# Kernel tuning notes

Measured on AMD Instinct MI355X. Metric: run time of the kernel, lower is better.

## Reference

```python
import jax, jax.numpy as jnp
import numpy as np

B, L, INPUT_DIM = 2, 2048, 512
D_MODEL, N_HEAD, MLP_HIDDEN = 1024, 16, 4096
CONTEXT_LENGTH = 2048
EPS = 1e-5


def _layer_norm(x, w, b):
    mu = jnp.mean(x, axis=-1, keepdims=True)
    var = jnp.mean(jnp.square(x - mu), axis=-1, keepdims=True)
    return (x - mu) * jax.lax.rsqrt(var + EPS) * w + b


def setup_inputs() -> dict:
    key = jax.random.key(0)
    ks = jax.random.split(key, 12)
    s = 0.02
    return {
        "x": jax.random.normal(ks[0], (B, L, INPUT_DIM), dtype=jnp.float32),
        "wte_w": jax.random.normal(ks[1], (INPUT_DIM, D_MODEL), dtype=jnp.float32) * s,
        "wte_b": jnp.zeros((D_MODEL,), dtype=jnp.float32),
        "wpe": jax.random.normal(ks[2], (CONTEXT_LENGTH, D_MODEL), dtype=jnp.float32) * s,
        "ln1_w": jnp.ones((D_MODEL,), dtype=jnp.float32),
        "ln1_b": jnp.zeros((D_MODEL,), dtype=jnp.float32),
        "kq_w": jax.random.normal(ks[3], (D_MODEL, 2 * D_MODEL), dtype=jnp.float32) * s,
        "kq_b": jnp.zeros((2 * D_MODEL,), dtype=jnp.float32),
        "v_w": jax.random.normal(ks[4], (D_MODEL, D_MODEL), dtype=jnp.float32) * s,
        "v_b": jnp.zeros((D_MODEL,), dtype=jnp.float32),
        "ao_w": jax.random.normal(ks[5], (D_MODEL, D_MODEL), dtype=jnp.float32) * s,
        "ao_b": jnp.zeros((D_MODEL,), dtype=jnp.float32),
        "ln2_w": jnp.ones((D_MODEL,), dtype=jnp.float32),
        "ln2_b": jnp.zeros((D_MODEL,), dtype=jnp.float32),
        "fc_w": jax.random.normal(ks[6], (D_MODEL, MLP_HIDDEN), dtype=jnp.float32) * s,
        "fc_b": jnp.zeros((MLP_HIDDEN,), dtype=jnp.float32),
        "proj_w": jax.random.normal(ks[7], (MLP_HIDDEN, INPUT_DIM), dtype=jnp.float32) * s,
        "proj_b": jnp.zeros((INPUT_DIM,), dtype=jnp.float32),
    }


def reference(x, wte_w, wte_b, wpe, ln1_w, ln1_b, kq_w, kq_b, v_w, v_b,
              ao_w, ao_b, ln2_w, ln2_b, fc_w, fc_b, proj_w, proj_b):
    b, l, _ = x.shape
    hd = D_MODEL // N_HEAD
    # token "embedding" (linear) + learnable positional embedding
    h = x @ wte_w + wte_b + wpe[:l]                      # [B, L, D]
    hn = _layer_norm(h, ln1_w, ln1_b)                    # ln_1
    # attention (kq fused linear -> split gives k first, then q)
    kq = hn @ kq_w + kq_b                                # [B, L, 2D]
    k, q = kq[..., :D_MODEL], kq[..., D_MODEL:]
    v = hn @ v_w + v_b
    q = q.reshape(b, l, N_HEAD, hd).transpose(0, 2, 1, 3)  # [B, H, L, hd]
    k = k.reshape(b, l, N_HEAD, hd).transpose(0, 2, 1, 3)
    v = v.reshape(b, l, N_HEAD, hd).transpose(0, 2, 1, 3)
    scale = 1.0 / jnp.sqrt(jnp.asarray(hd, dtype=q.dtype))
    scores = jnp.einsum('bhqd,bhkd->bhqk', q, k) * scale  # [B, H, L, L]
    causal = jnp.tril(jnp.ones((l, l), dtype=bool))
    scores = jnp.where(causal, scores, jnp.asarray(-jnp.inf, dtype=scores.dtype))
    attn = jax.nn.softmax(scores, axis=-1)
    o = jnp.einsum('bhqk,bhkd->bhqd', attn, v)            # [B, H, L, hd]
    o = o.transpose(0, 2, 1, 3).reshape(b, l, D_MODEL)
    o = o @ ao_w + ao_b
    attn_out = hn + o                                     # residual recorded by Block
    xo = _layer_norm(attn_out, ln2_w, ln2_b)              # ln_2
    # MLP head to input_dim (exact GELU, matching torch nn.GELU default)
    out = jax.nn.gelu(xo @ fc_w + fc_b, approximate=False) @ proj_w + proj_b
    return (out, attn_out)
```

## Files before the change

### kernel.cpp

```cpp
#include <hip/hip_runtime.h>
#include <hip/hip_bf16.h>
#include <cmath>

#define D_MODEL   1024
#define N_HEAD    16
#define HEAD_DIM  64
#define SEQ_LEN   2048
#define NBATCH    2
#define M_TOTAL   (NBATCH * SEQ_LEN)
#define IN_DIM    512
#define MLP_HID   4096

typedef __attribute__((ext_vector_type(8))) short short8;
typedef __attribute__((ext_vector_type(4))) short short4v;
typedef __attribute__((ext_vector_type(4))) float floatx4;

typedef const __attribute__((address_space(1))) void* gas_ptr;
typedef __attribute__((address_space(3))) void* las_ptr;

__device__ __forceinline__ void async_copy16(const void* g, void* l) {
  __builtin_amdgcn_global_load_lds((gas_ptr)g, (las_ptr)l, 16, 0, 0);
}


__global__ __launch_bounds__(256) void k_prep(const float* __restrict__ wte_w,
                                              const float* __restrict__ kq_w,
                                              const float* __restrict__ v_w,
                                              const float* __restrict__ ao_w,
                                              const float* __restrict__ fc_w,
                                              const float* __restrict__ proj_w,
                                              const float* __restrict__ x,
                                              __hip_bfloat16* __restrict__ wT,
                                              __hip_bfloat16* __restrict__ x_bf) {
  const int bid = blockIdx.x;
  const float* in; __hip_bfloat16* out; int K, N, local;
  if (bid < 512)        { in = wte_w;  out = wT;           K = IN_DIM;  N = D_MODEL;     local = bid;        }
  else if (bid < 2560)  { in = kq_w;   out = wT +  524288; K = D_MODEL; N = 2 * D_MODEL; local = bid - 512;  }
  else if (bid < 3584)  { in = v_w;    out = wT + 2621440; K = D_MODEL; N = D_MODEL;     local = bid - 2560; }
  else if (bid < 4608)  { in = ao_w;   out = wT + 3670016; K = D_MODEL; N = D_MODEL;     local = bid - 3584; }
  else if (bid < 8704)  { in = fc_w;   out = wT + 4718592; K = D_MODEL; N = MLP_HID;     local = bid - 4608; }
  else if (bid < 10752) { in = proj_w; out = wT + 8912896; K = MLP_HID; N = IN_DIM;      local = bid - 8704; }
  else {
    int i = (bid - 10752) * 256 + threadIdx.x;
    float4 v = ((const float4*)x)[i];
    short4v o;
    ((__hip_bfloat16*)&o)[0] = __float2bfloat16(v.x);
    ((__hip_bfloat16*)&o)[1] = __float2bfloat16(v.y);
    ((__hip_bfloat16*)&o)[2] = __float2bfloat16(v.z);
    ((__hip_bfloat16*)&o)[3] = __float2bfloat16(v.w);
    ((short4v*)x_bf)[i] = o;
    return;
  }
  __shared__ float tile[32][33];
  const int ntx = N >> 5;
  const int bx = local % ntx, by = local / ntx;
  const int n0 = bx * 32, k0 = by * 32;
  const int tx = threadIdx.x & 31, ty = threadIdx.x >> 5;
#pragma unroll
  for (int i = 0; i < 32; i += 8)
    tile[ty + i][tx] = in[(size_t)(k0 + ty + i) * N + n0 + tx];
  __syncthreads();
#pragma unroll
  for (int i = 0; i < 32; i += 8)
    out[(size_t)(n0 + ty + i) * K + k0 + tx] = __float2bfloat16(tile[tx][ty + i]);
}

__global__ __launch_bounds__(256) void k_reduce_proj(const __hip_bfloat16* __restrict__ part,
                                                     const float* __restrict__ bias,
                                                     float* __restrict__ out) {
  int i = blockIdx.x * 256 + threadIdx.x;
  const size_t SP = (size_t)M_TOTAL * IN_DIM / 4;
  float4 s = ((const float4*)bias)[i & (IN_DIM / 4 - 1)];
#pragma unroll
  for (int j = 0; j < 8; j++) {
    short4v v = ((const short4v*)part)[i + j * SP];
    s.x += __bfloat162float(((const __hip_bfloat16*)&v)[0]);
    s.y += __bfloat162float(((const __hip_bfloat16*)&v)[1]);
    s.z += __bfloat162float(((const __hip_bfloat16*)&v)[2]);
    s.w += __bfloat162float(((const __hip_bfloat16*)&v)[3]);
  }
  ((float4*)out)[i] = s;
}

__global__ __launch_bounds__(256) void k_transpose_v(const __hip_bfloat16* __restrict__ in,
                                                     __hip_bfloat16* __restrict__ out) {
  __shared__ __hip_bfloat16 t[64][72];
  int bh = blockIdx.y;
  int l0 = blockIdx.x * 64;
  in  += (size_t)bh * SEQ_LEN * HEAD_DIM;
  out += (size_t)bh * HEAD_DIM * SEQ_LEN;
  int tx = threadIdx.x & 7, ty = threadIdx.x >> 3;
#pragma unroll
  for (int i = 0; i < 64; i += 32) {
    short8 v = *(const short8*)(in + (size_t)(l0 + ty + i) * HEAD_DIM + tx * 8);
#pragma unroll
    for (int j = 0; j < 8; j++) t[ty + i][tx * 8 + j] = ((__hip_bfloat16*)&v)[j];
  }
  __syncthreads();
#pragma unroll
  for (int i = 0; i < 64; i += 32) {
    int d = ty + i;
    short8 o;
#pragma unroll
    for (int j = 0; j < 8; j++) ((__hip_bfloat16*)&o)[j] = t[tx * 8 + j][d];
    *(short8*)(out + (size_t)d * SEQ_LEN + l0 + tx * 8) = o;
  }
}


__global__ __launch_bounds__(256) void k_ln1_combine(const float* __restrict__ part,
                                                     const float* __restrict__ wb,
                                                     const float* __restrict__ wpe,
                                                     const float* __restrict__ lw,
                                                     const float* __restrict__ lb,
                                                     __hip_bfloat16* __restrict__ out_bf) {
  int row = blockIdx.x;
  int l = row & (SEQ_LEN - 1);
  float4 a = ((const float4*)(part + (size_t)row * D_MODEL))[threadIdx.x];
  float4 c = ((const float4*)(part + (size_t)(M_TOTAL + row) * D_MODEL))[threadIdx.x];
  float4 wb4 = ((const float4*)wb)[threadIdx.x];
  float4 pe4 = ((const float4*)(wpe + (size_t)l * D_MODEL))[threadIdx.x];
  float4 v;
  v.x = a.x + c.x + wb4.x + pe4.x;
  v.y = a.y + c.y + wb4.y + pe4.y;
  v.z = a.z + c.z + wb4.z + pe4.z;
  v.w = a.w + c.w + wb4.w + pe4.w;
  float s  = v.x + v.y + v.z + v.w;
  float sq = v.x * v.x + v.y * v.y + v.z * v.z + v.w * v.w;
#pragma unroll
  for (int o = 1; o < 64; o <<= 1) { s += __shfl_xor(s, o); sq += __shfl_xor(sq, o); }
  __shared__ float ss[4], ssq[4];
  int lane = threadIdx.x & 63, wv = threadIdx.x >> 6;
  if (lane == 0) { ss[wv] = s; ssq[wv] = sq; }
  __syncthreads();
  s  = ss[0] + ss[1] + ss[2] + ss[3];
  sq = ssq[0] + ssq[1] + ssq[2] + ssq[3];
  float mu  = s * (1.f / D_MODEL);
  float var = sq * (1.f / D_MODEL) - mu * mu;
  float rs  = rsqrtf(var + 1e-5f);
  float4 lw4 = ((const float4*)lw)[threadIdx.x];
  float4 lb4 = ((const float4*)lb)[threadIdx.x];
  size_t base = (size_t)row * D_MODEL + threadIdx.x * 4;
  out_bf[base + 0] = __float2bfloat16((v.x - mu) * rs * lw4.x + lb4.x);
  out_bf[base + 1] = __float2bfloat16((v.y - mu) * rs * lw4.y + lb4.y);
  out_bf[base + 2] = __float2bfloat16((v.z - mu) * rs * lw4.z + lb4.z);
  out_bf[base + 3] = __float2bfloat16((v.w - mu) * rs * lw4.w + lb4.w);
}

__global__ __launch_bounds__(256) void k_ln2_combine(const float* __restrict__ part,
                                                     const float* __restrict__ bias,
                                                     const __hip_bfloat16* __restrict__ hn,
                                                     const float* __restrict__ lw,
                                                     const float* __restrict__ lb,
                                                     float* __restrict__ attn_out,
                                                     __hip_bfloat16* __restrict__ out_bf) {
  int row = blockIdx.x;
  float4 a = ((const float4*)(part + (size_t)row * D_MODEL))[threadIdx.x];
  float4 c = ((const float4*)(part + (size_t)(M_TOTAL + row) * D_MODEL))[threadIdx.x];
  float4 b4 = ((const float4*)bias)[threadIdx.x];
  short4v h4 = ((const short4v*)(hn + (size_t)row * D_MODEL))[threadIdx.x];
  float4 v;
  v.x = a.x + c.x + b4.x + __bfloat162float(((const __hip_bfloat16*)&h4)[0]);
  v.y = a.y + c.y + b4.y + __bfloat162float(((const __hip_bfloat16*)&h4)[1]);
  v.z = a.z + c.z + b4.z + __bfloat162float(((const __hip_bfloat16*)&h4)[2]);
  v.w = a.w + c.w + b4.w + __bfloat162float(((const __hip_bfloat16*)&h4)[3]);
  ((float4*)(attn_out + (size_t)row * D_MODEL))[threadIdx.x] = v;
  float s  = v.x + v.y + v.z + v.w;
  float sq = v.x * v.x + v.y * v.y + v.z * v.z + v.w * v.w;
#pragma unroll
  for (int o = 1; o < 64; o <<= 1) { s += __shfl_xor(s, o); sq += __shfl_xor(sq, o); }
  __shared__ float ss[4], ssq[4];
  int lane = threadIdx.x & 63, wv = threadIdx.x >> 6;
  if (lane == 0) { ss[wv] = s; ssq[wv] = sq; }
  __syncthreads();
  s  = ss[0] + ss[1] + ss[2] + ss[3];
  sq = ssq[0] + ssq[1] + ssq[2] + ssq[3];
  float mu  = s * (1.f / D_MODEL);
  float var = sq * (1.f / D_MODEL) - mu * mu;
  float rs  = rsqrtf(var + 1e-5f);
  float4 lw4 = ((const float4*)lw)[threadIdx.x];
  float4 lb4 = ((const float4*)lb)[threadIdx.x];
  size_t base = (size_t)row * D_MODEL + threadIdx.x * 4;
  out_bf[base + 0] = __float2bfloat16((v.x - mu) * rs * lw4.x + lb4.x);
  out_bf[base + 1] = __float2bfloat16((v.y - mu) * rs * lw4.y + lb4.y);
  out_bf[base + 2] = __float2bfloat16((v.z - mu) * rs * lw4.z + lb4.z);
  out_bf[base + 3] = __float2bfloat16((v.w - mu) * rs * lw4.w + lb4.w);
}


struct KQVEpi {
  const float* kq_b; const float* v_b;
  __hip_bfloat16* kb; __hip_bfloat16* qb; __hip_bfloat16* vb;
  __device__ void operator()(int row, int col, float v) const {
    int b = row >> 11, l = row & (SEQ_LEN - 1);
    int which = col >> 10, c = col & (D_MODEL - 1);
    float t = v + ((which == 2) ? v_b[c] : kq_b[col]);
    if (which == 1) t *= 0.125f;
    int head = c >> 6, d = c & 63;
    __hip_bfloat16* dst = (which == 0) ? kb : (which == 1) ? qb : vb;
    dst[(((size_t)(b * N_HEAD + head) * SEQ_LEN) + l) * HEAD_DIM + d] = __float2bfloat16(t);
  }
};

struct FCEpi {
  const float* bias; __hip_bfloat16* act;
  __device__ void operator()(int row, int col, float v) const {
    float t = v + bias[col];
    float g = 0.5f * t * (1.f + erff(t * 0.70710678118654752f));
    act[(size_t)row * MLP_HID + col] = __float2bfloat16(g);
  }
};

struct PartEpi {
  float* part;
  __device__ void operator()(int row, int col, float v) const {
    part[(size_t)blockIdx.z * ((size_t)M_TOTAL * D_MODEL) + (size_t)row * D_MODEL + col] = v;
  }
};

struct PartBf16Epi {
  __hip_bfloat16* part;
  __device__ void operator()(int row, int col, float v) const {
    part[(size_t)blockIdx.z * ((size_t)M_TOTAL * IN_DIM) + (size_t)row * IN_DIM + col] =
        __float2bfloat16(v);
  }
};


template <class Epi>
__global__ __launch_bounds__(256) void k_gemm(const __hip_bfloat16* __restrict__ A,
                                              const __hip_bfloat16* __restrict__ Bt,
                                              int M, int N, int K, int Kchunk, Epi epi) {
  __shared__ __align__(16) short As[128 * 64];
  __shared__ __align__(16) short Bs[128 * 64];
  const int tid  = threadIdx.x;
  const int lane = tid & 63;
  const int w    = tid >> 6;
  const int wm   = (w >> 1) << 6;
  const int wn   = (w & 1) << 6;
  const int r    = lane & 15;
  const int quad = lane >> 4;
  const int m0 = blockIdx.y << 7;
  const int n0 = blockIdx.x << 7;
  const int koff = blockIdx.z * Kchunk;

  const __hip_bfloat16* pa[4];
  const __hip_bfloat16* pb[4];
#pragma unroll
  for (int j = 0; j < 4; j++) {
    int s = tid + j * 256;
    int row = s >> 3;
    int c = (s & 7) ^ (row & 7);
    pa[j] = A  + (size_t)(m0 + row) * K + (c << 3) + koff;
    pb[j] = Bt + (size_t)(n0 + row) * K + (c << 3) + koff;
  }

  floatx4 acc[4][4];
#pragma unroll
  for (int i = 0; i < 4; i++)
#pragma unroll
    for (int j = 0; j < 4; j++) acc[i][j] = (floatx4){0.f, 0.f, 0.f, 0.f};

  int aoff[2][4], boff[2][4];
#pragma unroll
  for (int kk = 0; kk < 2; kk++)
#pragma unroll
    for (int i = 0; i < 4; i++) {
      int pc = ((quad + (kk << 2)) ^ (r & 7)) << 3;
      aoff[kk][i] = (wm + i * 16 + r) * 64 + pc;
      boff[kk][i] = (wn + i * 16 + r) * 64 + pc;
    }

  for (int k0 = 0; k0 < Kchunk; k0 += 64) {
    __syncthreads();
#pragma unroll
    for (int j = 0; j < 4; j++) {
      async_copy16(pa[j] + k0, &As[(tid + j * 256) * 8]);
      async_copy16(pb[j] + k0, &Bs[(tid + j * 256) * 8]);
    }
    __syncthreads();
#pragma unroll
    for (int kk = 0; kk < 2; kk++) {
      short8 fa[4], fb[4];
#pragma unroll
      for (int i = 0; i < 4; i++) {
        fa[i] = *(const short8*)&As[aoff[kk][i]];
        fb[i] = *(const short8*)&Bs[boff[kk][i]];
      }
#pragma unroll
      for (int i = 0; i < 4; i++)
#pragma unroll
        for (int j = 0; j < 4; j++)
          acc[i][j] = __builtin_amdgcn_mfma_f32_16x16x32_bf16(fa[i], fb[j], acc[i][j], 0, 0, 0);
    }
  }

#pragma unroll
  for (int i = 0; i < 4; i++)
#pragma unroll
    for (int j = 0; j < 4; j++) {
      int row = m0 + wm + i * 16 + quad * 4;
      int col = n0 + wn + j * 16 + r;
#pragma unroll
      for (int t = 0; t < 4; t++) epi(row + t, col, acc[i][j][t]);
    }
}

template <class Epi>
static void launch_gemm(const __hip_bfloat16* A, const __hip_bfloat16* Bt,
                        int M, int N, int K, Epi epi, hipStream_t s) {
  dim3 grid(N / 128, M / 128, 1);
  k_gemm<Epi><<<grid, 256, 0, s>>>(A, Bt, M, N, K, K, epi);
}


#define STAGE_A(BUF, H, KT)                                                       \
  do {                                                                            \
    async_copy16(ga + (size_t)((H) * 128) * K + (KT) * 64,                        \
                 &As[BUF][(tid + (H) * 1024) * 8]);                               \
    async_copy16(ga + (size_t)((H) * 128 + 64) * K + (KT) * 64,                   \
                 &As[BUF][(tid + (H) * 1024 + 512) * 8]);                         \
  } while (0)

#define STAGE_B(BUF, H, KT)                                                       \
  do {                                                                            \
    async_copy16(gb + (size_t)((H) * 128) * K + (KT) * 64,                        \
                 &Bs[BUF][(tid + (H) * 1024) * 8]);                               \
    async_copy16(gb + (size_t)((H) * 128 + 64) * K + (KT) * 64,                   \
                 &Bs[BUF][(tid + (H) * 1024 + 512) * 8]);                         \
  } while (0)

#define MFMA_BLK(IO, JO, BFX)                                                     \
  _Pragma("unroll") for (int i = 0; i < 4; i++) {                                 \
    _Pragma("unroll") for (int j = 0; j < 2; j++) {                               \
      acc[(IO) + i][(JO) + j] = __builtin_amdgcn_mfma_f32_16x16x32_bf16(          \
          af[i][0], BFX[j][0], acc[(IO) + i][(JO) + j], 0, 0, 0);                 \
      acc[(IO) + i][(JO) + j] = __builtin_amdgcn_mfma_f32_16x16x32_bf16(          \
          af[i][1], BFX[j][1], acc[(IO) + i][(JO) + j], 0, 0, 0);                 \
    }                                                                             \
  }

#define GTILE(T, BUF)                                                             \
  {                                                                               \
    _Pragma("unroll") for (int i = 0; i < 4; i++) {                               \
      af[i][0] = *(const short8*)&As[BUF][arb[i] + pc0];                          \
      af[i][1] = *(const short8*)&As[BUF][arb[i] + pc1];                          \
    }                                                                             \
    _Pragma("unroll") for (int j = 0; j < 2; j++) {                               \
      bf0[j][0] = *(const short8*)&Bs[BUF][brb[j] + pc0];                         \
      bf0[j][1] = *(const short8*)&Bs[BUF][brb[j] + pc1];                         \
    }                                                                             \
    if ((T) + 1 < nt) { STAGE_A((BUF) ^ 1, 1, (T) + 1); }                         \
    __builtin_amdgcn_s_barrier();                                                 \
    asm volatile("s_waitcnt lgkmcnt(0)" ::: "memory");                            \
    __builtin_amdgcn_s_setprio(1);                                                \
    MFMA_BLK(0, 0, bf0)                                                           \
    __builtin_amdgcn_s_setprio(0);                                                \
    __builtin_amdgcn_s_barrier();                                                 \
    _Pragma("unroll") for (int j = 0; j < 2; j++) {                               \
      bf1[j][0] = *(const short8*)&Bs[BUF][brb[j] + 8192 + pc0];                  \
      bf1[j][1] = *(const short8*)&Bs[BUF][brb[j] + 8192 + pc1];                  \
    }                                                                             \
    if ((T) + 2 < nt) { STAGE_A(BUF, 0, (T) + 2); }                               \
    __builtin_amdgcn_s_barrier();                                                 \
    asm volatile("s_waitcnt lgkmcnt(0)" ::: "memory");                            \
    __builtin_amdgcn_s_setprio(1);                                                \
    MFMA_BLK(0, 2, bf1)                                                           \
    __builtin_amdgcn_s_setprio(0);                                                \
    __builtin_amdgcn_s_barrier();                                                 \
    _Pragma("unroll") for (int i = 0; i < 4; i++) {                               \
      af[i][0] = *(const short8*)&As[BUF][arb[i] + 8192 + pc0];                   \
      af[i][1] = *(const short8*)&As[BUF][arb[i] + 8192 + pc1];                   \
    }                                                                             \
    if ((T) + 2 < nt) { STAGE_B(BUF, 0, (T) + 2); }                               \
    __builtin_amdgcn_s_barrier();                                                 \
    asm volatile("s_waitcnt lgkmcnt(0)" ::: "memory");                            \
    __builtin_amdgcn_s_setprio(1);                                                \
    MFMA_BLK(4, 0, bf0)                                                           \
    __builtin_amdgcn_s_setprio(0);                                                \
    __builtin_amdgcn_s_barrier();                                                 \
    if ((T) + 2 < nt) { STAGE_B(BUF, 1, (T) + 2); }                               \
    __builtin_amdgcn_s_setprio(1);                                                \
    MFMA_BLK(4, 2, bf1)                                                           \
    __builtin_amdgcn_s_setprio(0);                                                \
    if ((T) + 2 < nt) {                                                           \
      asm volatile("s_waitcnt vmcnt(6)" ::: "memory");                            \
    } else {                                                                      \
      asm volatile("s_waitcnt vmcnt(0)" ::: "memory");                            \
    }                                                                             \
    __builtin_amdgcn_s_barrier();                                                 \
  }

template <class Epi>
__global__ __launch_bounds__(512, 2) void k_gemm256(const __hip_bfloat16* __restrict__ A,
                                                    const __hip_bfloat16* __restrict__ Bt,
                                                    int M, int N, int K, int Kchunk, Epi epi) {
  (void)M; (void)N;
  __shared__ __align__(16) short As[2][16384];
  __shared__ __align__(16) short Bs[2][16384];
  const int tid  = threadIdx.x;
  const int lane = tid & 63;
  const int w    = tid >> 6;
  const int wr   = w >> 2;
  const int wc   = w & 3;
  const int r    = lane & 15;
  const int quad = lane >> 4;
  const int m0 = blockIdx.y << 8;
  const int n0 = blockIdx.x << 8;
  const int koff = blockIdx.z * Kchunk;
  const int nt = Kchunk >> 6;

  const int sr = tid >> 3;
  const int sc = (tid & 7) ^ (sr & 7);
  const __hip_bfloat16* ga = A  + (size_t)(m0 + sr) * K + sc * 8 + koff;
  const __hip_bfloat16* gb = Bt + (size_t)(n0 + sr) * K + sc * 8 + koff;

  const int pc0 = ((quad    ) ^ (r & 7)) << 3;
  const int pc1 = ((quad + 4) ^ (r & 7)) << 3;
  int arb[4], brb[2];
#pragma unroll
  for (int i = 0; i < 4; i++) arb[i] = ((2 * i + wr) * 16 + r) * 64;
#pragma unroll
  for (int j = 0; j < 2; j++) brb[j] = ((4 * j + wc) * 16 + r) * 64;

  floatx4 acc[8][4];
#pragma unroll
  for (int i = 0; i < 8; i++)
#pragma unroll
    for (int j = 0; j < 4; j++) acc[i][j] = (floatx4){0.f, 0.f, 0.f, 0.f};
  short8 af[4][2], bf0[2][2], bf1[2][2];

  STAGE_A(0, 0, 0);
  STAGE_B(0, 0, 0);
  STAGE_B(0, 1, 0);
  STAGE_A(0, 1, 0);
  if (nt > 1) {
    STAGE_A(1, 0, 1);
    STAGE_B(1, 0, 1);
    STAGE_B(1, 1, 1);
    asm volatile("s_waitcnt vmcnt(6)" ::: "memory");
  } else {
    asm volatile("s_waitcnt vmcnt(0)" ::: "memory");
  }
  __builtin_amdgcn_s_barrier();

  for (int t = 0; t < nt; t += 2) {
    GTILE(t, 0)
    GTILE(t + 1, 1)
  }

#pragma unroll
  for (int i = 0; i < 8; i++) {
    int row = m0 + (2 * i + wr) * 16 + quad * 4;
#pragma unroll
    for (int j = 0; j < 4; j++) {
      int col = n0 + (4 * j + wc) * 16 + r;
#pragma unroll
      for (int tt = 0; tt < 4; tt++) epi(row + tt, col, acc[i][j][tt]);
    }
  }
}


#define PSTR 68

#define STAGE_KV(T, P)                                                         \
  do {                                                                         \
    async_copy16(kp + (size_t)((((T) << 6)) + srow) * HEAD_DIM + sg * 8,       \
                 &Ks[P][tid * 8]);                                             \
    async_copy16(vp + (size_t)srow * SEQ_LEN + ((T) << 6) + sg * 8,            \
                 &Vs[P][tid * 8]);                                             \
  } while (0)

#define ATILE(T, P)                                                            \
  {                                                                            \
    const int ts = (T) << 6;                                                   \
    if (ts < qend) {                                                           \
      _Pragma("unroll") for (int kt = 0; kt < 4; kt++) {                       \
        const int tss = ts + (kt << 4);                                        \
        short4v pk0;                                                           \
        if (tss < qend) {                                                      \
          const int krow = (kt << 4) + r;                                      \
          short8 a0 = *(const short8*)&Ks[P][(krow * 8 + (quad ^ sw)) * 8];    \
          short8 a1 = *(const short8*)&Ks[P][(krow * 8 + ((quad ^ sw) ^ 4)) * 8]; \
          floatx4 s0 = (floatx4){0.f, 0.f, 0.f, 0.f};                          \
          s0 = __builtin_amdgcn_mfma_f32_16x16x32_bf16(a0, qf0, s0, 0, 0, 0);  \
          s0 = __builtin_amdgcn_mfma_f32_16x16x32_bf16(a1, qf1, s0, 0, 0, 0);  \
          if (tss + 15 > qbw) {                                                \
            int off0 = qbw + r - tss;                                          \
            _Pragma("unroll") for (int tt = 0; tt < 4; tt++) {                 \
              int kl = (quad << 2) + tt;                                       \
              if (kl > off0) s0[tt] = -INFINITY;                               \
            }                                                                  \
          }                                                                    \
          _Pragma("unroll") for (int tt = 0; tt < 4; tt++) {                   \
            float e0 = __expf(s0[tt]); ls0 += e0;                              \
            ((__hip_bfloat16*)&pk0)[tt] = __float2bfloat16(e0);                \
          }                                                                    \
        } else {                                                               \
          pk0 = (short4v){0, 0, 0, 0};                                         \
        }                                                                      \
        *(short4v*)(pw + r * PSTR + (kt << 4) + (quad << 2)) = pk0;            \
      }                                                                        \
      __builtin_amdgcn_s_setprio(1);                                           \
      _Pragma("unroll") for (int c = 0; c < 2; c++) {                          \
        short8 pb0 = *(const short8*)(pw + r * PSTR + (c << 5) + (quad << 3)); \
        _Pragma("unroll") for (int fd = 0; fd < 4; fd++) {                     \
          const int vrow = (fd << 4) + r;                                      \
          short8 va = *(const short8*)&Vs[P][(vrow * 8 + (((c << 2) + quad) ^ sw)) * 8]; \
          of[fd] = __builtin_amdgcn_mfma_f32_16x16x32_bf16(va, pb0, of[fd], 0, 0, 0); \
        }                                                                      \
      }                                                                        \
      __builtin_amdgcn_s_setprio(0);                                           \
    }                                                                          \
    __builtin_amdgcn_s_barrier();                                              \
    if ((T) + 2 < ktiles) {                                                    \
      STAGE_KV((T) + 2, P);                                                    \
      asm volatile("s_waitcnt vmcnt(2)" ::: "memory");                         \
    } else {                                                                   \
      asm volatile("s_waitcnt vmcnt(0)" ::: "memory");                         \
    }                                                                          \
    __builtin_amdgcn_s_barrier();                                              \
    __builtin_amdgcn_sched_barrier(0);                                         \
  }

__global__ __launch_bounds__(512, 4) void k_flash_attn(const __hip_bfloat16* __restrict__ kb,
                                                       const __hip_bfloat16* __restrict__ qb,
                                                       const __hip_bfloat16* __restrict__ vtb,
                                                       __hip_bfloat16* __restrict__ ob) {
  __shared__ __align__(16) short Ks[2][64 * 64];
  __shared__ __align__(16) short Vs[2][64 * 64];
  __shared__ __align__(16) __hip_bfloat16 Pb[8][16 * PSTR];
  const int tid  = threadIdx.x;
  const int lane = tid & 63;
  const int w    = tid >> 6;
  const int r    = lane & 15;
  const int quad = lane >> 4;
  const int sw   = r & 7;
  const int bh    = blockIdx.x & 31;
  const int strip = (SEQ_LEN / 128 - 1) - (blockIdx.x >> 5);
  const int qb0   = strip << 7;
  const int qbw   = qb0 + (w << 4);
  const int qend  = qbw + 16;
  const int b = bh >> 4, h = bh & (N_HEAD - 1);

  const __hip_bfloat16* qp = qb  + ((size_t)bh * SEQ_LEN + qbw) * HEAD_DIM;
  const __hip_bfloat16* kp = kb  + (size_t)bh * SEQ_LEN * HEAD_DIM;
  const __hip_bfloat16* vp = vtb + (size_t)bh * HEAD_DIM * SEQ_LEN;
  __hip_bfloat16* pw = &Pb[w][0];

  short8 qf0 = *(const short8*)(qp + r * HEAD_DIM + quad * 8);
  short8 qf1 = *(const short8*)(qp + r * HEAD_DIM + quad * 8 + 32);

  floatx4 of[4];
#pragma unroll
  for (int i = 0; i < 4; i++) of[i] = (floatx4){0.f, 0.f, 0.f, 0.f};
  float ls0 = 0.f;

  const int srow = tid >> 3;
  const int sg = (tid & 7) ^ (srow & 7);

  const int ktiles = (qb0 + 128) >> 6;
  STAGE_KV(0, 0);
  STAGE_KV(1, 1);
  asm volatile("s_waitcnt vmcnt(2)" ::: "memory");
  __builtin_amdgcn_s_barrier();
  __builtin_amdgcn_sched_barrier(0);

  for (int t = 0; t < ktiles; t += 2) {
    ATILE(t, 0)
    ATILE(t + 1, 1)
  }

  ls0 += __shfl_xor(ls0, 16); ls0 += __shfl_xor(ls0, 32);
  float inv0 = 1.f / ls0;

  size_t orow = ((size_t)b * SEQ_LEN + qbw + r) * D_MODEL + (size_t)h * HEAD_DIM;
#pragma unroll
  for (int fd = 0; fd < 4; fd++) {
    short4v o4;
#pragma unroll
    for (int tt = 0; tt < 4; tt++)
      ((__hip_bfloat16*)&o4)[tt] = __float2bfloat16(of[fd][tt] * inv0);
    *(short4v*)(ob + orow + fd * 16 + quad * 4) = o4;
  }
}


extern "C" void kernel_launch(void* const* d_in, const int* in_sizes, int n_in,
                              void* d_out, int out_size, void* d_ws, size_t ws_size,
                              hipStream_t stream) {
  (void)in_sizes; (void)n_in; (void)out_size; (void)ws_size;
  const float* x      = (const float*)d_in[0];
  const float* wte_w  = (const float*)d_in[1];
  const float* wte_b  = (const float*)d_in[2];
  const float* wpe    = (const float*)d_in[3];
  const float* ln1_w  = (const float*)d_in[4];
  const float* ln1_b  = (const float*)d_in[5];
  const float* kq_w   = (const float*)d_in[6];
  const float* kq_b   = (const float*)d_in[7];
  const float* v_w    = (const float*)d_in[8];
  const float* v_b    = (const float*)d_in[9];
  const float* ao_w   = (const float*)d_in[10];
  const float* ao_b   = (const float*)d_in[11];
  const float* ln2_w  = (const float*)d_in[12];
  const float* ln2_b  = (const float*)d_in[13];
  const float* fc_w   = (const float*)d_in[14];
  const float* fc_b   = (const float*)d_in[15];
  const float* proj_w = (const float*)d_in[16];
  const float* proj_b = (const float*)d_in[17];

  float* out0     = (float*)d_out;
  float* attn_out = out0 + (size_t)M_TOTAL * IN_DIM;

  char* ws = (char*)d_ws;
  __hip_bfloat16* wT    = (__hip_bfloat16*)ws;
  __hip_bfloat16* x_bf  = (__hip_bfloat16*)(ws + 22 * 1048576);
  char* R1              = ws + 26 * 1048576;
  float* embed_part     = (float*)R1;
  float* ao_part        = (float*)R1;
  __hip_bfloat16* act   = (__hip_bfloat16*)R1;
  __hip_bfloat16* k_bf  = (__hip_bfloat16*)(ws + 58 * 1048576);
  __hip_bfloat16* q_bf  = (__hip_bfloat16*)(ws + 66 * 1048576);
  __hip_bfloat16* v_bf  = (__hip_bfloat16*)(ws + 74 * 1048576);
  __hip_bfloat16* vt_bf = (__hip_bfloat16*)(ws + 82 * 1048576);
  __hip_bfloat16* o_bf  = v_bf;
  __hip_bfloat16* hn_bf = (__hip_bfloat16*)(ws + 90 * 1048576);
  __hip_bfloat16* xo_bf = k_bf;
  __hip_bfloat16* proj_part = k_bf;

  __hip_bfloat16* wteT  = wT;
  __hip_bfloat16* kqvT  = wT +  524288;
  __hip_bfloat16* aoT   = wT + 3670016;
  __hip_bfloat16* fcT   = wT + 4718592;
  __hip_bfloat16* projT = wT + 8912896;

  k_prep<<<12800, 256, 0, stream>>>(wte_w, kq_w, v_w, ao_w, fc_w, proj_w, x, wT, x_bf);

  {
    dim3 grid(D_MODEL / 128, M_TOTAL / 128, 2);
    k_gemm<PartEpi><<<grid, 256, 0, stream>>>(x_bf, wteT, M_TOTAL, D_MODEL, IN_DIM, IN_DIM / 2,
                                              PartEpi{embed_part});
  }

  k_ln1_combine<<<M_TOTAL, 256, 0, stream>>>(embed_part, wte_b, wpe, ln1_w, ln1_b, hn_bf);

  launch_gemm(hn_bf, kqvT, M_TOTAL, 3 * D_MODEL, D_MODEL,
              KQVEpi{kq_b, v_b, k_bf, q_bf, v_bf}, stream);
  k_transpose_v<<<dim3(SEQ_LEN / 64, NBATCH * N_HEAD), 256, 0, stream>>>(v_bf, vt_bf);

  k_flash_attn<<<(SEQ_LEN / 128) * 32, 512, 0, stream>>>(k_bf, q_bf, vt_bf, o_bf);

  {
    dim3 grid(D_MODEL / 128, M_TOTAL / 128, 2);
    k_gemm<PartEpi><<<grid, 256, 0, stream>>>(o_bf, aoT, M_TOTAL, D_MODEL, D_MODEL, D_MODEL / 2,
                                              PartEpi{ao_part});
  }

  k_ln2_combine<<<M_TOTAL, 256, 0, stream>>>(ao_part, ao_b, hn_bf, ln2_w, ln2_b, attn_out, xo_bf);

  launch_gemm(xo_bf, fcT, M_TOTAL, MLP_HID, D_MODEL, FCEpi{fc_b, act}, stream);

  {
    dim3 grid(IN_DIM / 256, M_TOTAL / 256, 8);
    k_gemm256<PartBf16Epi><<<grid, 512, 0, stream>>>(act, projT, M_TOTAL, IN_DIM, MLP_HID,
                                                     MLP_HID / 8, PartBf16Epi{proj_part});
  }
  k_reduce_proj<<<M_TOTAL * IN_DIM / 4 / 256, 256, 0, stream>>>(proj_part, proj_b, out0);
}
```

Measured before the change: 386.8 us.

## Fuse V transpose into KQV GEMM epilogue and use 256-tile GEMM for FC

```diff
diff --git a/kernel.cpp b/kernel.cpp
--- a/kernel.cpp
+++ b/kernel.cpp
@@ -82,31 +82,6 @@
   ((float4*)out)[i] = s;
 }
 
-__global__ __launch_bounds__(256) void k_transpose_v(const __hip_bfloat16* __restrict__ in,
-                                                     __hip_bfloat16* __restrict__ out) {
-  __shared__ __hip_bfloat16 t[64][72];
-  int bh = blockIdx.y;
-  int l0 = blockIdx.x * 64;
-  in  += (size_t)bh * SEQ_LEN * HEAD_DIM;
-  out += (size_t)bh * HEAD_DIM * SEQ_LEN;
-  int tx = threadIdx.x & 7, ty = threadIdx.x >> 3;
-#pragma unroll
-  for (int i = 0; i < 64; i += 32) {
-    short8 v = *(const short8*)(in + (size_t)(l0 + ty + i) * HEAD_DIM + tx * 8);
-#pragma unroll
-    for (int j = 0; j < 8; j++) t[ty + i][tx * 8 + j] = ((__hip_bfloat16*)&v)[j];
-  }
-  __syncthreads();
-#pragma unroll
-  for (int i = 0; i < 64; i += 32) {
-    int d = ty + i;
-    short8 o;
-#pragma unroll
-    for (int j = 0; j < 8; j++) ((__hip_bfloat16*)&o)[j] = t[tx * 8 + j][d];
-    *(short8*)(out + (size_t)d * SEQ_LEN + l0 + tx * 8) = o;
-  }
-}
-
 
 __global__ __launch_bounds__(256) void k_ln1_combine(const float* __restrict__ part,
                                                      const float* __restrict__ wb,
@@ -190,39 +165,60 @@
 
 struct KQVEpi {
   const float* kq_b; const float* v_b;
-  __hip_bfloat16* kb; __hip_bfloat16* qb; __hip_bfloat16* vb;
-  __device__ void operator()(int row, int col, float v) const {
+  __hip_bfloat16* kb; __hip_bfloat16* qb; __hip_bfloat16* vt;
+  __device__ void operator()(int row, int col, const floatx4& v) const {
     int b = row >> 11, l = row & (SEQ_LEN - 1);
     int which = col >> 10, c = col & (D_MODEL - 1);
-    float t = v + ((which == 2) ? v_b[c] : kq_b[col]);
-    if (which == 1) t *= 0.125f;
     int head = c >> 6, d = c & 63;
-    __hip_bfloat16* dst = (which == 0) ? kb : (which == 1) ? qb : vb;
-    dst[(((size_t)(b * N_HEAD + head) * SEQ_LEN) + l) * HEAD_DIM + d] = __float2bfloat16(t);
+    if (which == 2) {
+      float bias = v_b[c];
+      short4v o;
+#pragma unroll
+      for (int t = 0; t < 4; t++)
+        ((__hip_bfloat16*)&o)[t] = __float2bfloat16(v[t] + bias);
+      *(short4v*)(vt + ((size_t)(b * N_HEAD + head) * HEAD_DIM + d) * SEQ_LEN + l) = o;
+    } else {
+      float bias = kq_b[col];
+      float scale = (which == 1) ? 0.125f : 1.f;
+      __hip_bfloat16* dst = (which == 0) ? kb : qb;
+#pragma unroll
+      for (int t = 0; t < 4; t++)
+        dst[((size_t)(b * N_HEAD + head) * SEQ_LEN + l + t) * HEAD_DIM + d] =
+            __float2bfloat16((v[t] + bias) * scale);
+    }
   }
 };
 
 struct FCEpi {
   const float* bias; __hip_bfloat16* act;
-  __device__ void operator()(int row, int col, float v) const {
-    float t = v + bias[col];
-    float g = 0.5f * t * (1.f + erff(t * 0.70710678118654752f));
-    act[(size_t)row * MLP_HID + col] = __float2bfloat16(g);
+  __device__ void operator()(int row, int col, const floatx4& v) const {
+    float bi = bias[col];
+#pragma unroll
+    for (int t = 0; t < 4; t++) {
+      float x = v[t] + bi;
+      float g = 0.5f * x * (1.f + erff(x * 0.70710678118654752f));
+      act[(size_t)(row + t) * MLP_HID + col] = __float2bfloat16(g);
+    }
   }
 };
 
 struct PartEpi {
   float* part;
-  __device__ void operator()(int row, int col, float v) const {
-    part[(size_t)blockIdx.z * ((size_t)M_TOTAL * D_MODEL) + (size_t)row * D_MODEL + col] = v;
+  __device__ void operator()(int row, int col, const floatx4& v) const {
+    float* p = part + (size_t)blockIdx.z * ((size_t)M_TOTAL * D_MODEL) +
+               (size_t)row * D_MODEL + col;
+#pragma unroll
+    for (int t = 0; t < 4; t++) p[(size_t)t * D_MODEL] = v[t];
   }
 };
 
 struct PartBf16Epi {
   __hip_bfloat16* part;
-  __device__ void operator()(int row, int col, float v) const {
-    part[(size_t)blockIdx.z * ((size_t)M_TOTAL * IN_DIM) + (size_t)row * IN_DIM + col] =
-        __float2bfloat16(v);
+  __device__ void operator()(int row, int col, const floatx4& v) const {
+    __hip_bfloat16* p = part + (size_t)blockIdx.z * ((size_t)M_TOTAL * IN_DIM) +
+                        (size_t)row * IN_DIM + col;
+#pragma unroll
+    for (int t = 0; t < 4; t++) p[(size_t)t * IN_DIM] = __float2bfloat16(v[t]);
   }
 };
 
@@ -298,12 +294,8 @@
 #pragma unroll
   for (int i = 0; i < 4; i++)
 #pragma unroll
-    for (int j = 0; j < 4; j++) {
-      int row = m0 + wm + i * 16 + quad * 4;
-      int col = n0 + wn + j * 16 + r;
-#pragma unroll
-      for (int t = 0; t < 4; t++) epi(row + t, col, acc[i][j][t]);
-    }
+    for (int j = 0; j < 4; j++)
+      epi(m0 + wm + i * 16 + quad * 4, n0 + wn + j * 16 + r, acc[i][j]);
 }
 
 template <class Epi>
@@ -450,15 +442,10 @@
   }
 
 #pragma unroll
-  for (int i = 0; i < 8; i++) {
-    int row = m0 + (2 * i + wr) * 16 + quad * 4;
-#pragma unroll
-    for (int j = 0; j < 4; j++) {
-      int col = n0 + (4 * j + wc) * 16 + r;
-#pragma unroll
-      for (int tt = 0; tt < 4; tt++) epi(row + tt, col, acc[i][j][tt]);
-    }
-  }
+  for (int i = 0; i < 8; i++)
+#pragma unroll
+    for (int j = 0; j < 4; j++)
+      epi(m0 + (2 * i + wr) * 16 + quad * 4, n0 + (4 * j + wc) * 16 + r, acc[i][j]);
 }
 
 
@@ -622,9 +609,8 @@
   __hip_bfloat16* act   = (__hip_bfloat16*)R1;
   __hip_bfloat16* k_bf  = (__hip_bfloat16*)(ws + 58 * 1048576);
   __hip_bfloat16* q_bf  = (__hip_bfloat16*)(ws + 66 * 1048576);
-  __hip_bfloat16* v_bf  = (__hip_bfloat16*)(ws + 74 * 1048576);
-  __hip_bfloat16* vt_bf = (__hip_bfloat16*)(ws + 82 * 1048576);
-  __hip_bfloat16* o_bf  = v_bf;
+  __hip_bfloat16* vt_bf = (__hip_bfloat16*)(ws + 74 * 1048576);
+  __hip_bfloat16* o_bf  = (__hip_bfloat16*)(ws + 82 * 1048576);
   __hip_bfloat16* hn_bf = (__hip_bfloat16*)(ws + 90 * 1048576);
   __hip_bfloat16* xo_bf = k_bf;
   __hip_bfloat16* proj_part = k_bf;
@@ -646,8 +632,7 @@
   k_ln1_combine<<<M_TOTAL, 256, 0, stream>>>(embed_part, wte_b, wpe, ln1_w, ln1_b, hn_bf);
 
   launch_gemm(hn_bf, kqvT, M_TOTAL, 3 * D_MODEL, D_MODEL,
-              KQVEpi{kq_b, v_b, k_bf, q_bf, v_bf}, stream);
-  k_transpose_v<<<dim3(SEQ_LEN / 64, NBATCH * N_HEAD), 256, 0, stream>>>(v_bf, vt_bf);
+              KQVEpi{kq_b, v_b, k_bf, q_bf, vt_bf}, stream);
 
   k_flash_attn<<<(SEQ_LEN / 128) * 32, 512, 0, stream>>>(k_bf, q_bf, vt_bf, o_bf);
 
@@ -659,7 +644,11 @@
 
   k_ln2_combine<<<M_TOTAL, 256, 0, stream>>>(ao_part, ao_b, hn_bf, ln2_w, ln2_b, attn_out, xo_bf);
 
-  launch_gemm(xo_bf, fcT, M_TOTAL, MLP_HID, D_MODEL, FCEpi{fc_b, act}, stream);
+  {
+    dim3 grid(MLP_HID / 256, M_TOTAL / 256, 1);
+    k_gemm256<FCEpi><<<grid, 512, 0, stream>>>(xo_bf, fcT, M_TOTAL, MLP_HID, D_MODEL, D_MODEL,
+                                               FCEpi{fc_b, act});
+  }
 
   {
     dim3 grid(IN_DIM / 256, M_TOTAL / 256, 8);
```

Measured after the change: 358.3 us. 1.08x faster.
